# Optimization experiments

Measured on AMD Instinct MI355X. Metric: run time of the kernel, lower is better.

The kernel has to match this reference:

```python
import jax, jax.numpy as jnp
import numpy as np

N, M, E, H = 4096, 16384, 512, 8
D = E // H  # head dim = 64


def _rms(x, g, eps=1e-6):
    return x * jax.lax.rsqrt(jnp.mean(jnp.square(x), axis=-1, keepdims=True) + eps) * g


def _split(x):
    # (rows, E) -> (rows, H, D)
    return x.reshape(x.shape[0], H, D)


def _sdpa(q, k, v):
    # Faithful to the source layout: SDPA on (rows, H, D) tensors, i.e. per-row
    # attention over the H heads (tiny HxH softmax per node).
    s = jnp.einsum('nhd,ngd->nhg', q, k) / jnp.sqrt(jnp.asarray(D, q.dtype))
    a = jax.nn.softmax(s, axis=-1)
    return jnp.einsum('nhg,ngd->nhd', a, v).reshape(-1, E)


def setup_inputs() -> dict:
    key = jax.random.key(0)
    ks = jax.random.split(key, 25)
    w = lambda k, s, sc: jax.random.normal(k, s, dtype=jnp.float32) * sc
    se = 1.0 / np.sqrt(E)   # Linear(E, E) init scale
    sm = 1.0 / np.sqrt(M)   # Linear(M, N) init scale
    inp = {
        'x_node': jax.random.normal(ks[0], (N, E), dtype=jnp.float32),
        'x_edge': jax.random.normal(ks[1], (M, E), dtype=jnp.float32),
        # sparse-ish binary adjacency, avg degree ~8
        'adj': (jax.random.uniform(ks[2], (N, N)) < 0.002).astype(jnp.float32),
        # per-branch QKV weights (4 separate MultiHeadAttention modules)
        'Wq_hh': w(ks[3], (E, E), se), 'Wk_hh': w(ks[4], (E, E), se), 'Wv_hh': w(ks[5], (E, E), se),
        'Wq_ee': w(ks[6], (E, E), se), 'Wk_ee': w(ks[7], (E, E), se), 'Wv_ee': w(ks[8], (E, E), se),
        'Wq_he': w(ks[9], (E, E), se), 'Wk_he': w(ks[10], (E, E), se), 'Wv_he': w(ks[11], (E, E), se),
        'Wq_eh': w(ks[12], (E, E), se), 'Wk_eh': w(ks[13], (E, E), se), 'Wv_eh': w(ks[14], (E, E), se),
        # shape_proj (edges -> nodes) weights, one per module that uses it
        'Wp1_he': w(ks[15], (N, M), sm),
        'Wp1_eh': w(ks[16], (N, M), sm),
        'Wp1_ee': w(ks[17], (N, M), sm),
        # RMSNorm gains
        'g_n': jnp.ones((E,), jnp.float32),
        'g_e': jnp.ones((E,), jnp.float32),
        'g2': jnp.ones((E,), jnp.float32),
        # FeedForward
        'Wf1': w(ks[18], (E, 4 * E), se), 'bf1': jnp.zeros((4 * E,), jnp.float32),
        'Wf2': w(ks[19], (4 * E, E), 1.0 / np.sqrt(4 * E)), 'bf2': jnp.zeros((E,), jnp.float32),
    }
    return inp


def reference(x_node, x_edge, adj,
              Wq_hh, Wk_hh, Wv_hh, Wq_ee, Wk_ee, Wv_ee,
              Wq_he, Wk_he, Wv_he, Wq_eh, Wk_eh, Wv_eh,
              Wp1_he, Wp1_eh, Wp1_ee,
              g_n, g_e, g2, Wf1, bf1, Wf2, bf2):
    h = _rms(x_node, g_n)   # (N, E)
    e = _rms(x_edge, g_e)   # (M, E)

    # hh: adjacency injected into the node query branch
    q = jnp.einsum('nm,mhd->nhd', adj, _split(h @ Wq_hh))
    out_hh = _sdpa(q, _split(h @ Wk_hh), _split(h @ Wv_hh))

    # ee: edge queries/keys projected to node rows via shape_proj
    q = jnp.einsum('nm,mhd->nhd', Wp1_ee, _split(e @ Wq_ee))
    k = jnp.einsum('nm,mhd->nhd', Wp1_ee, _split(e @ Wk_ee))
    out_ee = _sdpa(q, k, _split(h @ Wv_ee))

    # eh: edge query projected to node rows, node key
    q = jnp.einsum('nm,mhd->nhd', Wp1_eh, _split(e @ Wq_eh))
    out_eh = _sdpa(q, _split(h @ Wk_eh), _split(h @ Wv_eh))

    # he: node query, edge key projected to node rows
    k = jnp.einsum('nm,mhd->nhd', Wp1_he, _split(e @ Wk_he))
    out_he = _sdpa(_split(h @ Wq_he), k, _split(h @ Wv_he))

    x = out_hh + out_ee + out_eh + out_he          # (N, E)
    y = _rms(x, g2)
    return jax.nn.gelu(y @ Wf1 + bf1, approximate=False) @ Wf2 + bf2
```

## Files before the change

kernel.cpp:

```cpp
#include <hip/hip_runtime.h>
#include <cstdint>


typedef unsigned short u16;
typedef __bf16 bf16x8 __attribute__((ext_vector_type(8)));
typedef float f32x4 __attribute__((ext_vector_type(4)));

__device__ __forceinline__ u16 f2bf(float f) {
    unsigned u = __float_as_uint(f);
    return (u16)((u + 0x7fffu + ((u >> 16) & 1u)) >> 16);
}
__device__ __forceinline__ float bf2f(u16 u) { return __uint_as_float(((unsigned)u) << 16); }
__device__ __forceinline__ float gelu_exact(float x) {
    return 0.5f * x * (1.0f + erff(x * 0.70710678118654752f));
}

__device__ __forceinline__ void gload_lds16(const u16* g, u16* l) {
    __builtin_amdgcn_global_load_lds(
        (const __attribute__((address_space(1))) unsigned int*)(uintptr_t)g,
        (__attribute__((address_space(3))) unsigned int*)(unsigned int)(uintptr_t)l,
        16, 0, 0);
}

__device__ __forceinline__ void swz_block(int& bx, int& by, int& bz) {
    const int nx = gridDim.x, ny = gridDim.y;
    const int nwg = nx * ny * gridDim.z;
    int lin = blockIdx.x + nx * (blockIdx.y + ny * blockIdx.z);
    const int chunk = nwg >> 3;
    lin = (lin & 7) * chunk + (lin >> 3);
    bx = lin % nx;
    lin /= nx;
    by = lin % ny;
    bz = lin / ny;
}

__global__ __launch_bounds__(256) void cvt_f32_bf16(const float* __restrict__ in,
                                                    u16* __restrict__ out, size_t n8) {
    size_t i = (size_t)blockIdx.x * 256 + threadIdx.x;
    size_t stride = (size_t)gridDim.x * 256;
    for (; i < n8; i += stride) {
        float4 a = ((const float4*)in)[i * 2];
        float4 b = ((const float4*)in)[i * 2 + 1];
        u16 r[8] = {f2bf(a.x), f2bf(a.y), f2bf(a.z), f2bf(a.w),
                    f2bf(b.x), f2bf(b.y), f2bf(b.z), f2bf(b.w)};
        ((uint4*)out)[i] = *(const uint4*)r;
    }
}

__global__ __launch_bounds__(256) void transpose_cvt(const float* __restrict__ in,
                                                     u16* __restrict__ out, int R, int C) {
    __shared__ float tile[32][33];
    int c0 = blockIdx.x * 32, r0 = blockIdx.y * 32;
    int tx = threadIdx.x & 31, ty = threadIdx.x >> 5;
#pragma unroll
    for (int i = 0; i < 4; ++i)
        tile[ty + i * 8][tx] = in[(size_t)(r0 + ty + i * 8) * C + c0 + tx];
    __syncthreads();
#pragma unroll
    for (int i = 0; i < 4; ++i)
        out[(size_t)(c0 + ty + i * 8) * R + r0 + tx] = f2bf(tile[tx][ty + i * 8]);
}

struct W12 { const float* in[12]; u16* out[12]; };
__global__ __launch_bounds__(256) void transpose_cvt12(W12 w) {
    __shared__ float tile[32][33];
    const float* in = w.in[blockIdx.z];
    u16* out = w.out[blockIdx.z];
    int c0 = blockIdx.x * 32, r0 = blockIdx.y * 32;
    int tx = threadIdx.x & 31, ty = threadIdx.x >> 5;
#pragma unroll
    for (int i = 0; i < 4; ++i)
        tile[ty + i * 8][tx] = in[(size_t)(r0 + ty + i * 8) * 512 + c0 + tx];
    __syncthreads();
#pragma unroll
    for (int i = 0; i < 4; ++i)
        out[(size_t)(c0 + ty + i * 8) * 512 + r0 + tx] = f2bf(tile[tx][ty + i * 8]);
}

__global__ __launch_bounds__(256) void transpose_u16(const u16* __restrict__ in,
                                                     u16* __restrict__ out, int R, int C) {
    __shared__ u16 tile[32][34];
    int c0 = blockIdx.x * 32, r0 = blockIdx.y * 32;
    int tx = threadIdx.x & 31, ty = threadIdx.x >> 5;
#pragma unroll
    for (int i = 0; i < 4; ++i)
        tile[ty + i * 8][tx] = in[(size_t)(r0 + ty + i * 8) * C + c0 + tx];
    __syncthreads();
#pragma unroll
    for (int i = 0; i < 4; ++i)
        out[(size_t)(c0 + ty + i * 8) * R + r0 + tx] = tile[tx][ty + i * 8];
}

__global__ __launch_bounds__(256) void rmsnorm_bf16(const float* __restrict__ x,
                                                    const float* __restrict__ g,
                                                    u16* __restrict__ out) {
    int row = blockIdx.x, tid = threadIdx.x;
    const float* xr = x + (size_t)row * 512;
    float2 v = *(const float2*)(xr + tid * 2);
    float ss = v.x * v.x + v.y * v.y;
#pragma unroll
    for (int o = 32; o; o >>= 1) ss += __shfl_down(ss, o);
    __shared__ float red[4];
    if ((tid & 63) == 0) red[tid >> 6] = ss;
    __syncthreads();
    float tot = red[0] + red[1] + red[2] + red[3];
    float rs = rsqrtf(tot * (1.0f / 512.0f) + 1e-6f);
    unsigned pack = (unsigned)f2bf(v.x * rs * g[tid * 2]) |
                    ((unsigned)f2bf(v.y * rs * g[tid * 2 + 1]) << 16);
    ((unsigned*)out)[(size_t)row * 256 + tid] = pack;
}

template <int MODE>
__device__ __forceinline__ void gemm_tile_body(const u16* __restrict__ A,
                                               const u16* __restrict__ Bt,
                                               int N, int K, int k_begin, int k_end,
                                               int rowStart, int colStart,
                                               void* __restrict__ C,
                                               const float* __restrict__ bias) {
    __shared__ u16 Asm[128 * 32];
    __shared__ u16 Bsm[128 * 32];
    const int tid = threadIdx.x;
    const int wave = tid >> 6, lane = tid & 63;
    const int wr = wave >> 1, wc = wave & 1;

    f32x4 acc[4][4];
#pragma unroll
    for (int m = 0; m < 4; ++m)
#pragma unroll
        for (int n = 0; n < 4; ++n) acc[m][n] = f32x4{0.f, 0.f, 0.f, 0.f};

    const int off0 = (wave * 2 + 0) * 1024 + lane * 16;
    const int off1 = (wave * 2 + 1) * 1024 + lane * 16;
    const int r0 = off0 >> 6, k0e = (off0 & 63) >> 1;
    const int r1 = off1 >> 6, k1e = (off1 & 63) >> 1;
    const size_t Arow0 = (size_t)(rowStart + r0) * K + k0e;
    const size_t Arow1 = (size_t)(rowStart + r1) * K + k1e;
    const size_t Brow0 = (size_t)(colStart + r0) * K + k0e;
    const size_t Brow1 = (size_t)(colStart + r1) * K + k1e;
    u16* As0 = &Asm[(wave * 2 + 0) * 512];
    u16* As1 = &Asm[(wave * 2 + 1) * 512];
    u16* Bs0 = &Bsm[(wave * 2 + 0) * 512];
    u16* Bs1 = &Bsm[(wave * 2 + 1) * 512];

    const int rsel = lane & 15, kselb = (lane >> 4) * 8;

    for (int kk = k_begin; kk < k_end; kk += 32) {
        gload_lds16(A + Arow0 + kk, As0);
        gload_lds16(A + Arow1 + kk, As1);
        gload_lds16(Bt + Brow0 + kk, Bs0);
        gload_lds16(Bt + Brow1 + kk, Bs1);
        __syncthreads();
        bf16x8 aF[4], bF[4];
#pragma unroll
        for (int m = 0; m < 4; ++m)
            aF[m] = *(const bf16x8*)&Asm[(wr * 64 + m * 16 + rsel) * 32 + kselb];
#pragma unroll
        for (int n = 0; n < 4; ++n)
            bF[n] = *(const bf16x8*)&Bsm[(wc * 64 + n * 16 + rsel) * 32 + kselb];
#pragma unroll
        for (int m = 0; m < 4; ++m)
#pragma unroll
            for (int n = 0; n < 4; ++n)
                acc[m][n] = __builtin_amdgcn_mfma_f32_16x16x32_bf16(aF[m], bF[n], acc[m][n], 0, 0, 0);
        __syncthreads();
    }

    const int cq = (lane >> 4) * 4, cr = lane & 15;
#pragma unroll
    for (int m = 0; m < 4; ++m) {
#pragma unroll
        for (int n = 0; n < 4; ++n) {
            int col = colStart + wc * 64 + n * 16 + cr;
#pragma unroll
            for (int j = 0; j < 4; ++j) {
                int row = rowStart + wr * 64 + m * 16 + cq + j;
                float v = acc[m][n][j];
                if constexpr (MODE == 0) {
                    ((u16*)C)[(size_t)row * N + col] = f2bf(v);
                } else if constexpr (MODE == 1) {
                    v = gelu_exact(v + bias[col]);
                    ((u16*)C)[(size_t)row * N + col] = f2bf(v);
                } else if constexpr (MODE == 2) {
                    ((float*)C)[(size_t)row * N + col] = v + bias[col];
                } else {
                    if (bias) v += bias[col];
                    atomicAdd(&((float*)C)[(size_t)row * N + col], v);
                }
            }
        }
    }
}

template <int MODE>
__global__ __launch_bounds__(256, 2) void gemm_bt(const u16* __restrict__ A,
                                                  const u16* __restrict__ Bt,
                                                  void* __restrict__ C,
                                                  const float* __restrict__ bias,
                                                  int N, int K, int kLen) {
    int bx, by, bz;
    swz_block(bx, by, bz);
    const float* bb = (MODE == 3) ? ((bz == 0) ? bias : nullptr) : bias;
    int kb = bz * kLen;
    gemm_tile_body<MODE>(A, Bt, N, K, kb, kb + kLen, by * 128, bx * 128, C, bb);
}

struct Small12 { const u16* A[12]; const u16* W[12]; u16* C[12]; };
__global__ __launch_bounds__(256, 2) void gemm_small12(Small12 s) {
    int bx, by, bz;
    swz_block(bx, by, bz);
    gemm_tile_body<0>(s.A[bz], s.W[bz], 512, 512, 0, 512, by * 128, bx * 128, s.C[bz], nullptr);
}

struct Big3 { const float* A[3]; };
__global__ __launch_bounds__(256, 2) void gemm_f32a(Big3 ba, const u16* __restrict__ Bt,
                                                    float* __restrict__ C0, int K,
                                                    int zPerMat, int kLen) {
    __shared__ u16 Asm[128 * 32];
    __shared__ u16 Bsm[128 * 32];
    int bx, by, bz;
    swz_block(bx, by, bz);
    const int m = bz / zPerMat, ks = bz - m * zPerMat;
    const float* __restrict__ A = ba.A[m];
    float* __restrict__ C = C0 + (size_t)m * (4096 * 512);
    const int rowStart = by * 128, colStart = bx * 128;
    const int k0 = ks * kLen, kEnd = k0 + kLen;

    const int tid = threadIdx.x;
    const int wave = tid >> 6, lane = tid & 63;
    const int wr = wave >> 1, wc = wave & 1;

    f32x4 acc[4][4];
#pragma unroll
    for (int mm = 0; mm < 4; ++mm)
#pragma unroll
        for (int n = 0; n < 4; ++n) acc[mm][n] = f32x4{0.f, 0.f, 0.f, 0.f};

    const int r = tid >> 1, half = tid & 1;
    const float4* Ap4 = (const float4*)(A + (size_t)(rowStart + r) * K + half * 16);
    const int sw = (r & 7) << 4;
    u16* aw0 = (u16*)((char*)Asm + (((r * 64 + half * 32) ^ sw)));
    u16* aw1 = (u16*)((char*)Asm + (((r * 64 + half * 32 + 16) ^ sw)));

    const int off0 = (wave * 2 + 0) * 1024 + lane * 16;
    const int off1 = (wave * 2 + 1) * 1024 + lane * 16;
    const int br0 = off0 >> 6, bk0 = (off0 & 63) >> 1;
    const int br1 = off1 >> 6, bk1 = (off1 & 63) >> 1;
    const u16* Bp0 = Bt + (size_t)(colStart + br0) * K + bk0;
    const u16* Bp1 = Bt + (size_t)(colStart + br1) * K + bk1;
    u16* Bs0 = &Bsm[(wave * 2 + 0) * 512];
    u16* Bs1 = &Bsm[(wave * 2 + 1) * 512];

    const int rsel = lane & 15, ksel = lane >> 4;

    float4 a0, a1, a2, a3;
    {
        const float4* p = Ap4 + (k0 >> 2);
        a0 = p[0]; a1 = p[1]; a2 = p[2]; a3 = p[3];
    }
    for (int kk = k0; kk < kEnd; kk += 32) {
        gload_lds16(Bp0 + kk, Bs0);
        gload_lds16(Bp1 + kk, Bs1);
        bf16x8 c0, c1;
        c0[0] = (__bf16)a0.x; c0[1] = (__bf16)a0.y; c0[2] = (__bf16)a0.z; c0[3] = (__bf16)a0.w;
        c0[4] = (__bf16)a1.x; c0[5] = (__bf16)a1.y; c0[6] = (__bf16)a1.z; c0[7] = (__bf16)a1.w;
        c1[0] = (__bf16)a2.x; c1[1] = (__bf16)a2.y; c1[2] = (__bf16)a2.z; c1[3] = (__bf16)a2.w;
        c1[4] = (__bf16)a3.x; c1[5] = (__bf16)a3.y; c1[6] = (__bf16)a3.z; c1[7] = (__bf16)a3.w;
        *(bf16x8*)aw0 = c0;
        *(bf16x8*)aw1 = c1;
        if (kk + 32 < kEnd) {
            const float4* p = Ap4 + ((kk + 32) >> 2);
            a0 = p[0]; a1 = p[1]; a2 = p[2]; a3 = p[3];
        }
        __syncthreads();
        bf16x8 aF[4], bF[4];
#pragma unroll
        for (int mm = 0; mm < 4; ++mm) {
            int R = wr * 64 + mm * 16 + rsel;
            aF[mm] = *(const bf16x8*)((char*)Asm + ((R * 64 + ksel * 16) ^ ((R & 7) << 4)));
        }
#pragma unroll
        for (int n = 0; n < 4; ++n)
            bF[n] = *(const bf16x8*)&Bsm[(wc * 64 + n * 16 + rsel) * 32 + ksel * 8];
#pragma unroll
        for (int mm = 0; mm < 4; ++mm)
#pragma unroll
            for (int n = 0; n < 4; ++n)
                acc[mm][n] = __builtin_amdgcn_mfma_f32_16x16x32_bf16(aF[mm], bF[n], acc[mm][n], 0, 0, 0);
        __syncthreads();
    }

    const int cq = (lane >> 4) * 4, cr = lane & 15;
#pragma unroll
    for (int mm = 0; mm < 4; ++mm)
#pragma unroll
        for (int n = 0; n < 4; ++n) {
            int col = colStart + wc * 64 + n * 16 + cr;
#pragma unroll
            for (int j = 0; j < 4; ++j) {
                int row = rowStart + wr * 64 + mm * 16 + cq + j;
                atomicAdd(&C[(size_t)row * 512 + col], acc[mm][n][j]);
            }
        }
}

struct SP12 { const u16* p[12]; };
__global__ __launch_bounds__(256) void sdpa_fused(SP12 sp, const float* __restrict__ g2,
                                                  u16* __restrict__ y) {
    __shared__ float qb[4][8][65], kb[4][8][65], vb[4][8][65];
    __shared__ float aw[4][64];
    __shared__ float red[4];
    const int n = blockIdx.x, tid = threadIdx.x;
    const size_t base = (size_t)n * 512;
    const int e0 = tid * 2, hs = e0 >> 6, ds = e0 & 63;

#pragma unroll
    for (int br = 0; br < 4; ++br) {
        unsigned u;
        u = *(const unsigned*)(sp.p[br * 3 + 0] + base + e0);
        qb[br][hs][ds] = bf2f(u & 0xffffu); qb[br][hs][ds + 1] = bf2f(u >> 16);
        u = *(const unsigned*)(sp.p[br * 3 + 1] + base + e0);
        kb[br][hs][ds] = bf2f(u & 0xffffu); kb[br][hs][ds + 1] = bf2f(u >> 16);
        u = *(const unsigned*)(sp.p[br * 3 + 2] + base + e0);
        vb[br][hs][ds] = bf2f(u & 0xffffu); vb[br][hs][ds + 1] = bf2f(u >> 16);
    }
    __syncthreads();

    const int b = tid >> 6, h = (tid >> 3) & 7, g = tid & 7;
    float s = 0.f;
    const float* qr = &qb[b][h][0];
    const float* kr = &kb[b][g][0];
#pragma unroll
    for (int j = 0; j < 64; ++j) s += qr[j] * kr[j];
    s *= 0.125f;
    float mx = s;
#pragma unroll
    for (int o = 1; o < 8; o <<= 1) mx = fmaxf(mx, __shfl_xor(mx, o));
    float p = expf(s - mx);
    float sm = p;
#pragma unroll
    for (int o = 1; o < 8; o <<= 1) sm += __shfl_xor(sm, o);
    aw[b][(h << 3) | g] = p / sm;
    __syncthreads();

    float o0 = 0.f, o1 = 0.f;
#pragma unroll
    for (int bb = 0; bb < 4; ++bb)
#pragma unroll
        for (int gg = 0; gg < 8; ++gg) {
            float a = aw[bb][(hs << 3) | gg];
            o0 += a * vb[bb][gg][ds];
            o1 += a * vb[bb][gg][ds + 1];
        }

    float ss = o0 * o0 + o1 * o1;
#pragma unroll
    for (int o = 32; o; o >>= 1) ss += __shfl_down(ss, o);
    if ((tid & 63) == 0) red[tid >> 6] = ss;
    __syncthreads();
    float tot = red[0] + red[1] + red[2] + red[3];
    float rs = rsqrtf(tot * (1.0f / 512.0f) + 1e-6f);
    unsigned pack = (unsigned)f2bf(o0 * rs * g2[e0]) | ((unsigned)f2bf(o1 * rs * g2[e0 + 1]) << 16);
    ((unsigned*)y)[(size_t)n * 256 + tid] = pack;
}

extern "C" void kernel_launch(void* const* d_in, const int* in_sizes, int n_in,
                              void* d_out, int out_size, void* d_ws, size_t ws_size,
                              hipStream_t stream) {
    (void)in_sizes; (void)n_in; (void)out_size; (void)ws_size;
    const int N = 4096, M = 16384, E = 512;

    const float* x_node = (const float*)d_in[0];
    const float* x_edge = (const float*)d_in[1];
    const float* adj    = (const float*)d_in[2];
    const float* Wp1_he = (const float*)d_in[15];
    const float* Wp1_eh = (const float*)d_in[16];
    const float* Wp1_ee = (const float*)d_in[17];
    const float* g_n = (const float*)d_in[18];
    const float* g_e = (const float*)d_in[19];
    const float* g2  = (const float*)d_in[20];
    const float* Wf1 = (const float*)d_in[21];
    const float* bf1 = (const float*)d_in[22];
    const float* Wf2 = (const float*)d_in[23];
    const float* bf2 = (const float*)d_in[24];

    char* p = (char*)d_ws;
    auto alloc = [&](size_t b) { char* r = p; p += (b + 255) & ~(size_t)255; return r; };
    const size_t NP = (size_t)N * E;
    const size_t WSZ = (size_t)E * E;
    u16* h    = (u16*)alloc(NP * 2);
    u16* hT   = (u16*)alloc(NP * 2);
    u16* e    = (u16*)alloc((size_t)M * E * 2);
    u16* eT   = (u16*)alloc((size_t)M * E * 2);
    u16* Wt   = (u16*)alloc(12 * WSZ * 2);
    u16* Wf1T = (u16*)alloc((size_t)2048 * 512 * 2);
    u16* Wf2T = (u16*)alloc((size_t)512 * 2048 * 2);
    float* F4 = (float*)alloc(4 * NP * 4);
    u16* P4b  = (u16*)alloc(4 * NP * 2);
    u16* S12  = (u16*)alloc(12 * NP * 2);
    u16* y    = (u16*)alloc(NP * 2);
    u16* t    = (u16*)alloc((size_t)N * 2048 * 2);

    W12 w12;
    for (int i = 0; i < 12; ++i) { w12.in[i] = (const float*)d_in[3 + i]; w12.out[i] = Wt + i * WSZ; }
    transpose_cvt12<<<dim3(16, 16, 12), 256, 0, stream>>>(w12);
    transpose_cvt<<<dim3(64, 16), 256, 0, stream>>>(Wf1, Wf1T, 512, 2048);
    transpose_cvt<<<dim3(16, 64), 256, 0, stream>>>(Wf2, Wf2T, 2048, 512);

    rmsnorm_bf16<<<N, 256, 0, stream>>>(x_node, g_n, h);
    rmsnorm_bf16<<<M, 256, 0, stream>>>(x_edge, g_e, e);
    transpose_u16<<<dim3(16, 128), 256, 0, stream>>>(h, hT, N, 512);
    transpose_u16<<<dim3(16, 512), 256, 0, stream>>>(e, eT, M, 512);

    hipMemsetAsync(F4, 0, 4 * NP * 4, stream);
    Big3 bp; bp.A[0] = Wp1_ee; bp.A[1] = Wp1_eh; bp.A[2] = Wp1_he;
    gemm_f32a<<<dim3(4, 32, 12), 256, 0, stream>>>(bp, eT, F4, M, 4, 4096);
    Big3 badj; badj.A[0] = adj; badj.A[1] = adj; badj.A[2] = adj;
    gemm_f32a<<<dim3(4, 32, 2), 256, 0, stream>>>(badj, hT, F4 + 3 * NP, N, 2, 2048);
    cvt_f32_bf16<<<2048, 256, 0, stream>>>(F4, P4b, 4 * NP / 8);
    const u16* Peeb = P4b + 0 * NP;
    const u16* Pehb = P4b + 1 * NP;
    const u16* Pheb = P4b + 2 * NP;
    const u16* Ahb  = P4b + 3 * NP;

    Small12 sb;
    const u16* aList[12] = {Ahb, h, h, Peeb, Peeb, h, Pehb, h, h, h, Pheb, h};
    const int wList[12]  = {0, 1, 2, 3, 4, 5, 9, 10, 11, 6, 7, 8};
    for (int i = 0; i < 12; ++i) {
        sb.A[i] = aList[i];
        sb.W[i] = Wt + wList[i] * WSZ;
        sb.C[i] = S12 + i * NP;
    }
    gemm_small12<<<dim3(4, 32, 12), 256, 0, stream>>>(sb);

    SP12 sp;
    for (int i = 0; i < 12; ++i) sp.p[i] = S12 + i * NP;
    sdpa_fused<<<N, 256, 0, stream>>>(sp, g2, y);

    gemm_bt<1><<<dim3(16, 32, 1), 256, 0, stream>>>(y, Wf1T, t, bf1, 2048, 512, 512);
    hipMemsetAsync(d_out, 0, NP * 4, stream);
    gemm_bt<3><<<dim3(4, 32, 2), 256, 0, stream>>>(t, Wf2T, d_out, bf2, 512, 2048, 1024);
}
```

Baseline: 671.5 us.

## Replace dense adjacency GEMM with ballot-based sparse SpMM and swizzle LDS layouts

Replaces the dense adj @ h GEMM (and the hT transpose it needed) with a per-row sparse kernel. Each wave ballots nonzero entries of one adjacency row and accumulates only the matching h rows. Separately, every bf16 producer now writes with an XOR swizzle on 16-byte chunks, and the GEMM fragment reads apply the matching swizzle, to cut LDS bank conflicts. The sparse path still reads the full fp32 adjacency but skips the matmul FLOPs; the swizzle must stay consistent across all producers and consumers.

```diff
diff --git a/kernel.cpp b/kernel.cpp
--- a/kernel.cpp
+++ b/kernel.cpp
@@ -34,6 +34,7 @@
     bz = lin / ny;
 }
 
+template <bool SWZ>
 __global__ __launch_bounds__(256) void cvt_f32_bf16(const float* __restrict__ in,
                                                     u16* __restrict__ out, size_t n8) {
     size_t i = (size_t)blockIdx.x * 256 + threadIdx.x;
@@ -43,7 +44,9 @@
         float4 b = ((const float4*)in)[i * 2 + 1];
         u16 r[8] = {f2bf(a.x), f2bf(a.y), f2bf(a.z), f2bf(a.w),
                     f2bf(b.x), f2bf(b.y), f2bf(b.z), f2bf(b.w)};
-        ((uint4*)out)[i] = *(const uint4*)r;
+        size_t o = i;
+        if constexpr (SWZ) o = (i & ~(size_t)63) | ((i & 63) ^ ((i >> 6) & 3));
+        ((uint4*)out)[o] = *(const uint4*)r;
     }
 }
 
@@ -57,8 +60,10 @@
         tile[ty + i * 8][tx] = in[(size_t)(r0 + ty + i * 8) * C + c0 + tx];
     __syncthreads();
 #pragma unroll
-    for (int i = 0; i < 4; ++i)
-        out[(size_t)(c0 + ty + i * 8) * R + r0 + tx] = f2bf(tile[tx][ty + i * 8]);
+    for (int i = 0; i < 4; ++i) {
+        int orow = c0 + ty + i * 8;
+        out[(size_t)orow * R + ((r0 + tx) ^ ((orow & 3) << 3))] = f2bf(tile[tx][ty + i * 8]);
+    }
 }
 
 struct W12 { const float* in[12]; u16* out[12]; };
@@ -73,8 +78,10 @@
         tile[ty + i * 8][tx] = in[(size_t)(r0 + ty + i * 8) * 512 + c0 + tx];
     __syncthreads();
 #pragma unroll
-    for (int i = 0; i < 4; ++i)
-        out[(size_t)(c0 + ty + i * 8) * 512 + r0 + tx] = f2bf(tile[tx][ty + i * 8]);
+    for (int i = 0; i < 4; ++i) {
+        int orow = c0 + ty + i * 8;
+        out[(size_t)orow * 512 + ((r0 + tx) ^ ((orow & 3) << 3))] = f2bf(tile[tx][ty + i * 8]);
+    }
 }
 
 __global__ __launch_bounds__(256) void transpose_u16(const u16* __restrict__ in,
@@ -87,10 +94,13 @@
         tile[ty + i * 8][tx] = in[(size_t)(r0 + ty + i * 8) * C + c0 + tx];
     __syncthreads();
 #pragma unroll
-    for (int i = 0; i < 4; ++i)
-        out[(size_t)(c0 + ty + i * 8) * R + r0 + tx] = tile[tx][ty + i * 8];
-}
-
+    for (int i = 0; i < 4; ++i) {
+        int orow = c0 + ty + i * 8;
+        out[(size_t)orow * R + ((r0 + tx) ^ ((orow & 3) << 3))] = tile[tx][ty + i * 8];
+    }
+}
+
+template <bool SWZ>
 __global__ __launch_bounds__(256) void rmsnorm_bf16(const float* __restrict__ x,
                                                     const float* __restrict__ g,
                                                     u16* __restrict__ out) {
@@ -107,7 +117,37 @@
     float rs = rsqrtf(tot * (1.0f / 512.0f) + 1e-6f);
     unsigned pack = (unsigned)f2bf(v.x * rs * g[tid * 2]) |
                     ((unsigned)f2bf(v.y * rs * g[tid * 2 + 1]) << 16);
-    ((unsigned*)out)[(size_t)row * 256 + tid] = pack;
+    int o32 = SWZ ? (tid ^ ((row & 3) << 2)) : tid;
+    ((unsigned*)out)[(size_t)row * 256 + o32] = pack;
+}
+
+__global__ __launch_bounds__(256) void adj_spmm(const float* __restrict__ adj,
+                                                const u16* __restrict__ h,
+                                                u16* __restrict__ out) {
+    const int wave = threadIdx.x >> 6, lane = threadIdx.x & 63;
+    const int n = blockIdx.x * 4 + wave;
+    const float* arow = adj + (size_t)n * 4096;
+    float acc[8] = {0.f, 0.f, 0.f, 0.f, 0.f, 0.f, 0.f, 0.f};
+    for (int j = 0; j < 64; ++j) {
+        float v = arow[j * 64 + lane];
+        unsigned long long mask = __ballot(v != 0.0f);
+        while (mask) {
+            int bit = __ffsll((long long)mask) - 1;
+            mask &= mask - 1;
+            int m = j * 64 + bit;
+            float w = __shfl(v, bit);
+            int cs = (lane & ~3) | ((lane & 3) ^ (m & 3));
+            uint4 q = *(const uint4*)(h + (size_t)m * 512 + cs * 8);
+            const u16* qu = (const u16*)&q;
+#pragma unroll
+            for (int t = 0; t < 8; ++t) acc[t] += w * bf2f(qu[t]);
+        }
+    }
+    int co = (lane & ~3) | ((lane & 3) ^ (n & 3));
+    u16 r[8];
+#pragma unroll
+    for (int t = 0; t < 8; ++t) r[t] = f2bf(acc[t]);
+    *(uint4*)(out + (size_t)n * 512 + co * 8) = *(const uint4*)r;
 }
 
 template <int MODE>
@@ -142,7 +182,8 @@
     u16* Bs0 = &Bsm[(wave * 2 + 0) * 512];
     u16* Bs1 = &Bsm[(wave * 2 + 1) * 512];
 
-    const int rsel = lane & 15, kselb = (lane >> 4) * 8;
+    const int rsel = lane & 15, ksel = lane >> 4;
+    const int fsw = ((ksel ^ (rsel & 3)) << 3);
 
     for (int kk = k_begin; kk < k_end; kk += 32) {
         gload_lds16(A + Arow0 + kk, As0);
@@ -153,10 +194,10 @@
         bf16x8 aF[4], bF[4];
 #pragma unroll
         for (int m = 0; m < 4; ++m)
-            aF[m] = *(const bf16x8*)&Asm[(wr * 64 + m * 16 + rsel) * 32 + kselb];
+            aF[m] = *(const bf16x8*)&Asm[(wr * 64 + m * 16 + rsel) * 32 + fsw];
 #pragma unroll
         for (int n = 0; n < 4; ++n)
-            bF[n] = *(const bf16x8*)&Bsm[(wc * 64 + n * 16 + rsel) * 32 + kselb];
+            bF[n] = *(const bf16x8*)&Bsm[(wc * 64 + n * 16 + rsel) * 32 + fsw];
 #pragma unroll
         for (int m = 0; m < 4; ++m)
 #pragma unroll
@@ -179,9 +220,7 @@
                     ((u16*)C)[(size_t)row * N + col] = f2bf(v);
                 } else if constexpr (MODE == 1) {
                     v = gelu_exact(v + bias[col]);
-                    ((u16*)C)[(size_t)row * N + col] = f2bf(v);
-                } else if constexpr (MODE == 2) {
-                    ((float*)C)[(size_t)row * N + col] = v + bias[col];
+                    ((u16*)C)[(size_t)row * N + (col ^ ((row & 3) << 3))] = f2bf(v);
                 } else {
                     if (bias) v += bias[col];
                     atomicAdd(&((float*)C)[(size_t)row * N + col], v);
@@ -251,6 +290,7 @@
     u16* Bs1 = &Bsm[(wave * 2 + 1) * 512];
 
     const int rsel = lane & 15, ksel = lane >> 4;
+    const int fsw = ((ksel ^ (rsel & 3)) << 3);
 
     float4 a0, a1, a2, a3;
     {
@@ -280,7 +320,7 @@
         }
 #pragma unroll
         for (int n = 0; n < 4; ++n)
-            bF[n] = *(const bf16x8*)&Bsm[(wc * 64 + n * 16 + rsel) * 32 + ksel * 8];
+            bF[n] = *(const bf16x8*)&Bsm[(wc * 64 + n * 16 + rsel) * 32 + fsw];
 #pragma unroll
         for (int mm = 0; mm < 4; ++mm)
 #pragma unroll
@@ -360,7 +400,7 @@
     float tot = red[0] + red[1] + red[2] + red[3];
     float rs = rsqrtf(tot * (1.0f / 512.0f) + 1e-6f);
     unsigned pack = (unsigned)f2bf(o0 * rs * g2[e0]) | ((unsigned)f2bf(o1 * rs * g2[e0 + 1]) << 16);
-    ((unsigned*)y)[(size_t)n * 256 + tid] = pack;
+    ((unsigned*)y)[(size_t)n * 256 + (tid ^ ((n & 3) << 2))] = pack;
 }
 
 extern "C" void kernel_launch(void* const* d_in, const int* in_sizes, int n_in,
@@ -388,14 +428,14 @@
     const size_t NP = (size_t)N * E;
     const size_t WSZ = (size_t)E * E;
     u16* h    = (u16*)alloc(NP * 2);
-    u16* hT   = (u16*)alloc(NP * 2);
     u16* e    = (u16*)alloc((size_t)M * E * 2);
     u16* eT   = (u16*)alloc((size_t)M * E * 2);
     u16* Wt   = (u16*)alloc(12 * WSZ * 2);
     u16* Wf1T = (u16*)alloc((size_t)2048 * 512 * 2);
     u16* Wf2T = (u16*)alloc((size_t)512 * 2048 * 2);
-    float* F4 = (float*)alloc(4 * NP * 4);
-    u16* P4b  = (u16*)alloc(4 * NP * 2);
+    float* F3 = (float*)alloc(3 * NP * 4);
+    u16* P3b  = (u16*)alloc(3 * NP * 2);
+    u16* Ahb  = (u16*)alloc(NP * 2);
     u16* S12  = (u16*)alloc(12 * NP * 2);
     u16* y    = (u16*)alloc(NP * 2);
     u16* t    = (u16*)alloc((size_t)N * 2048 * 2);
@@ -406,21 +446,18 @@
     transpose_cvt<<<dim3(64, 16), 256, 0, stream>>>(Wf1, Wf1T, 512, 2048);
     transpose_cvt<<<dim3(16, 64), 256, 0, stream>>>(Wf2, Wf2T, 2048, 512);
 
-    rmsnorm_bf16<<<N, 256, 0, stream>>>(x_node, g_n, h);
-    rmsnorm_bf16<<<M, 256, 0, stream>>>(x_edge, g_e, e);
-    transpose_u16<<<dim3(16, 128), 256, 0, stream>>>(h, hT, N, 512);
+    rmsnorm_bf16<true><<<N, 256, 0, stream>>>(x_node, g_n, h);
+    rmsnorm_bf16<false><<<M, 256, 0, stream>>>(x_edge, g_e, e);
     transpose_u16<<<dim3(16, 512), 256, 0, stream>>>(e, eT, M, 512);
-
-    hipMemsetAsync(F4, 0, 4 * NP * 4, stream);
+    adj_spmm<<<1024, 256, 0, stream>>>(adj, h, Ahb);
+
+    hipMemsetAsync(F3, 0, 3 * NP * 4, stream);
     Big3 bp; bp.A[0] = Wp1_ee; bp.A[1] = Wp1_eh; bp.A[2] = Wp1_he;
-    gemm_f32a<<<dim3(4, 32, 12), 256, 0, stream>>>(bp, eT, F4, M, 4, 4096);
-    Big3 badj; badj.A[0] = adj; badj.A[1] = adj; badj.A[2] = adj;
-    gemm_f32a<<<dim3(4, 32, 2), 256, 0, stream>>>(badj, hT, F4 + 3 * NP, N, 2, 2048);
-    cvt_f32_bf16<<<2048, 256, 0, stream>>>(F4, P4b, 4 * NP / 8);
-    const u16* Peeb = P4b + 0 * NP;
-    const u16* Pehb = P4b + 1 * NP;
-    const u16* Pheb = P4b + 2 * NP;
-    const u16* Ahb  = P4b + 3 * NP;
+    gemm_f32a<<<dim3(4, 32, 12), 256, 0, stream>>>(bp, eT, F3, M, 4, 4096);
+    cvt_f32_bf16<true><<<2048, 256, 0, stream>>>(F3, P3b, 3 * NP / 8);
+    const u16* Peeb = P3b + 0 * NP;
+    const u16* Pehb = P3b + 1 * NP;
+    const u16* Pheb = P3b + 2 * NP;
 
     Small12 sb;
     const u16* aList[12] = {Ahb, h, h, Peeb, Peeb, h, Pehb, h, h, h, Pheb, h};
```

After: 638.5 us. -4.9%, faster.
